# Performance work log

Hardware: AMD Instinct MI355X
Metric: run time of the kernel (lower is better)

Reference implementation:

```python
import jax, jax.numpy as jnp
import numpy as np

EPS = 1e-5
SCALE_MIN, SCALE_MAX = 0.6, 1.0


def _layer_norm(x):
    m = jnp.mean(x, axis=-1, keepdims=True)
    v = jnp.mean((x - m) ** 2, axis=-1, keepdims=True)
    return (x - m) / jnp.sqrt(v + EPS)


def _scan_dir(seq, A, Bp, Cp, D, W_in, W_out, snr_scale):
    """seq: [B, L, C] -> [B, L, C]. Diagonal SSM recurrence h = A*h + B*u."""
    Bsz, L, C = seq.shape
    N = A.shape[0]
    seq = _layer_norm(seq)
    u = jnp.einsum('blc,nc->bln', seq, W_in)                 # input_proj, [B,L,N]
    A_base = jnp.tanh(A)[None, :]                            # [1,N]
    s = jnp.clip(snr_scale, 0.0, 1.0)[:, None]               # [B,1]
    scale = SCALE_MIN + (SCALE_MAX - SCALE_MIN) * s
    Ad = jnp.clip(A_base * scale, -0.99, 0.99)               # [B,N]
    Bu = Bp[None, None, :] * u                               # [B,L,N]

    def step(h, bu_t):
        h = Ad * h + bu_t
        return h, h

    h0 = jnp.zeros((Bsz, N), dtype=seq.dtype)
    _, hs = jax.lax.scan(step, h0, jnp.swapaxes(Bu, 0, 1))   # hs: [L,B,N]
    hs = jnp.swapaxes(hs, 0, 1)                              # [B,L,N]
    y_state = Cp[None, None, :] * hs
    y = jnp.einsum('bln,cn->blc', y_state, W_out)            # output_proj
    return y + D[None, None, :] * seq


def _forward(x, snr_scale, A, Bparam, Cparam, D, W_in, W_out):
    Bsz, H, W, C = x.shape
    L = H * W
    if L > 4000:
        x = _layer_norm(x)
    # row scans
    seq_row = x.reshape(Bsz, L, C)
    y_row_f = _scan_dir(seq_row, A, Bparam, Cparam, D, W_in, W_out, snr_scale)
    y_row_b = _scan_dir(seq_row[:, ::-1, :], A, Bparam, Cparam, D, W_in, W_out, snr_scale)
    y_row = 0.5 * (y_row_f + y_row_b[:, ::-1, :])
    y_row = y_row.reshape(Bsz, H, W, C)
    # column scans
    x_col = jnp.transpose(x, (0, 2, 1, 3))                   # [B,W,H,C]
    seq_col = x_col.reshape(Bsz, L, C)
    y_col_f = _scan_dir(seq_col, A, Bparam, Cparam, D, W_in, W_out, snr_scale)
    y_col_b = _scan_dir(seq_col[:, ::-1, :], A, Bparam, Cparam, D, W_in, W_out, snr_scale)
    y_col = 0.5 * (y_col_f + y_col_b[:, ::-1, :])
    y_col = jnp.transpose(y_col.reshape(Bsz, W, H, C), (0, 2, 1, 3))
    return 0.5 * (y_row + y_col)


def setup_inputs() -> dict:
    key = jax.random.key(0)
    k = jax.random.split(key, 4)
    Bsz, H, W, C, N = 8, 64, 64, 256, 64
    x = jax.random.normal(k[0], (Bsz, H, W, C), dtype=jnp.float32)
    snr_scale = jax.random.uniform(k[1], (Bsz,), dtype=jnp.float32)
    A = -0.5 * jnp.ones((N,), dtype=jnp.float32)
    Bparam = 0.5 * jnp.ones((N,), dtype=jnp.float32)
    Cparam = 0.5 * jnp.ones((N,), dtype=jnp.float32)
    D = jnp.zeros((C,), dtype=jnp.float32)
    # nn.Linear default init: U(-1/sqrt(fan_in), 1/sqrt(fan_in))
    W_in = jax.random.uniform(k[2], (N, C), dtype=jnp.float32,
                              minval=-1.0 / np.sqrt(C), maxval=1.0 / np.sqrt(C))
    W_out = jax.random.uniform(k[3], (C, N), dtype=jnp.float32,
                               minval=-1.0 / np.sqrt(N), maxval=1.0 / np.sqrt(N))
    return {"x": x, "snr_scale": snr_scale, "A": A, "Bparam": Bparam,
            "Cparam": Cparam, "D": D, "W_in": W_in, "W_out": W_out}


def reference(x, snr_scale, A, Bparam, Cparam, D, W_in, W_out):
    return _forward(x, snr_scale, A, Bparam, Cparam, D, W_in, W_out)
```

## Files before the change

kernel.cpp:

```cpp
#include <hip/hip_runtime.h>
#include <hip/hip_bf16.h>
#include <math.h>

#define Bsz 8
#define Hh 64
#define Ww 64
#define Cc 256
#define Nn 64
#define Ll 4096
#define EPSf 1e-5f

typedef __bf16 v8bf __attribute__((ext_vector_type(8)));
typedef float  f32x4 __attribute__((ext_vector_type(4)));

__device__ __forceinline__ float ad_val(float a, float snr) {
    float s = fminf(fmaxf(snr, 0.f), 1.f);
    float scale = 0.6f + 0.4f * s;
    float v = tanhf(a) * scale;
    return fminf(fmaxf(v, -0.99f), 0.99f);
}

__global__ __launch_bounds__(256) void k0_weights(
    const float* __restrict__ Win, const float* __restrict__ Wout,
    const float* __restrict__ Bp, const float* __restrict__ Cp,
    __bf16* __restrict__ Wh, __bf16* __restrict__ Wl,
    __bf16* __restrict__ Woh, __bf16* __restrict__ Wol,
    float* __restrict__ WB)
{
    const int t = threadIdx.x;
    const int blk = blockIdx.x;
    if (blk < 4) {
        for (int idx = blk * 512 + t; idx < blk * 512 + 512; idx += 256) {
            int tile = idx >> 6, lane = idx & 63;
            int kt = tile >> 2, nt = tile & 3;
            int q = lane >> 4, n = nt * 16 + (lane & 15);
            #pragma unroll
            for (int j = 0; j < 8; ++j) {
                int k = kt * 32 + q * 8 + j;
                float w = Win[n * Cc + k];
                __bf16 h = (__bf16)w;
                Wh[idx * 8 + j] = h;
                Wl[idx * 8 + j] = (__bf16)(w - (float)h);
            }
        }
    } else if (blk < 8) {
        for (int idx = (blk - 4) * 512 + t; idx < (blk - 4) * 512 + 512; idx += 256) {
            int tile = idx >> 6, lane = idx & 63;
            int kt = tile >> 4, ntg = tile & 15;
            int q = lane >> 4, c = ntg * 16 + (lane & 15);
            #pragma unroll
            for (int j = 0; j < 8; ++j) {
                int k = kt * 32 + q * 8 + j;
                float w = Wout[c * Nn + k] * 0.25f * Cp[k];
                __bf16 h = (__bf16)w;
                Woh[idx * 8 + j] = h;
                Wol[idx * 8 + j] = (__bf16)(w - (float)h);
            }
        }
    } else {
        __shared__ float wtmp[256];
        int n = t >> 2, qd = t & 3;
        float s = 0.f;
        const float* wr = Win + (long)n * Cc + qd * 64;
        for (int i = 0; i < 64; ++i) s += wr[i];
        wtmp[t] = s;
        __syncthreads();
        if (t < 64)
            WB[t] = (wtmp[t*4] + wtmp[t*4+1] + wtmp[t*4+2] + wtmp[t*4+3]) * Bp[t];
    }
}

__global__ __launch_bounds__(256) void k1_ln_gemm(
    const float* __restrict__ x, const __bf16* __restrict__ Wh,
    const __bf16* __restrict__ Wl, const float* __restrict__ Bp,
    const float* __restrict__ WB, const float* __restrict__ A,
    const float* __restrict__ snr,
    float* __restrict__ Bu, float* __restrict__ E,
    float* __restrict__ Mst, float* __restrict__ Sst)
{
    __shared__ float tile[64 * 68];
    __shared__ float pfs[4][64], pbs[4][64];
    const int t = threadIdx.x;
    const int lane = t & 63;
    const int wv = __builtin_amdgcn_readfirstlane(t >> 6);
    const long pbase = (long)blockIdx.x * 64;
    const float* xt = x + pbase * Cc;

    const int q = lane >> 4;
    const int mi = lane & 15;
    const float* xa = xt + (long)(wv * 16 + mi) * Cc + q * 8;

    float4 axv[16];
    #pragma unroll
    for (int kt = 0; kt < 8; ++kt) {
        axv[kt * 2]     = *(const float4*)(xa + kt * 32);
        axv[kt * 2 + 1] = *(const float4*)(xa + kt * 32 + 4);
    }

    f32x4 acc[4];
    #pragma unroll
    for (int nt = 0; nt < 4; ++nt) acc[nt] = (f32x4){0.f, 0.f, 0.f, 0.f};
    float sacc = 0.f, qacc = 0.f;

    #pragma unroll
    for (int kt = 0; kt < 8; ++kt) {
        float4 a0 = axv[kt * 2];
        float4 a1 = axv[kt * 2 + 1];
        float av[8] = {a0.x, a0.y, a0.z, a0.w, a1.x, a1.y, a1.z, a1.w};
        v8bf ah, al;
        #pragma unroll
        for (int j = 0; j < 8; ++j) {
            sacc += av[j];
            qacc = fmaf(av[j], av[j], qacc);
            __bf16 h = (__bf16)av[j];
            ah[j] = h;
            al[j] = (__bf16)(av[j] - (float)h);
        }
        #pragma unroll
        for (int nt = 0; nt < 4; ++nt) {
            v8bf bh = *(const v8bf*)(Wh + ((long)(kt * 4 + nt) * 64 + lane) * 8);
            v8bf bl = *(const v8bf*)(Wl + ((long)(kt * 4 + nt) * 64 + lane) * 8);
            acc[nt] = __builtin_amdgcn_mfma_f32_16x16x32_bf16(ah, bh, acc[nt], 0, 0, 0);
            acc[nt] = __builtin_amdgcn_mfma_f32_16x16x32_bf16(al, bh, acc[nt], 0, 0, 0);
            acc[nt] = __builtin_amdgcn_mfma_f32_16x16x32_bf16(ah, bl, acc[nt], 0, 0, 0);
        }
    }

    sacc += __shfl_xor(sacc, 16);
    qacc += __shfl_xor(qacc, 16);
    sacc += __shfl_xor(sacc, 32);
    qacc += __shfl_xor(qacc, 32);
    float m_row = sacc * (1.f/256.f);
    float var = fmaxf(qacc * (1.f/256.f) - m_row * m_row, 0.f);
    float r1 = rsqrtf(var + EPSf);
    float v2 = var / (var + EPSf);
    float sc_row = r1 * rsqrtf(v2 + EPSf);
    if (lane < 16) {
        Mst[pbase + wv * 16 + mi] = m_row;
        Sst[pbase + wv * 16 + mi] = sc_row;
    }

    #pragma unroll
    for (int nt = 0; nt < 4; ++nt) {
        int n = nt * 16 + mi;
        float bpn = Bp[n];
        float wbn = WB[n];
        #pragma unroll
        for (int reg = 0; reg < 4; ++reg) {
            int p = wv * 16 + q * 4 + reg;
            float m = __shfl(m_row, q * 4 + reg);
            float s = __shfl(sc_row, q * 4 + reg);
            float val = s * (acc[nt][reg] * bpn - m * wbn);
            Bu[(pbase + p) * Nn + n] = val;
            tile[p * 68 + n] = val;
        }
    }
    __syncthreads();

    const int nn = t & 63;
    const int seg = t >> 6;
    const int bb = blockIdx.x >> 6;
    const int jj = blockIdx.x & 63;
    const float Adv = ad_val(A[nn], snr[bb]);

    float vv[16];
    #pragma unroll
    for (int k = 0; k < 16; ++k) vv[k] = tile[(seg * 16 + k) * 68 + nn];
    float f = 0.f, bw = 0.f;
    #pragma unroll
    for (int k = 0; k < 16; ++k) f = fmaf(Adv, f, vv[k]);
    #pragma unroll
    for (int k = 15; k >= 0; --k) bw = fmaf(Adv, bw, vv[k]);
    pfs[seg][nn] = f;
    pbs[seg][nn] = bw;
    __syncthreads();

    if (t < 64) {
        float Ad16 = Adv * Adv;
        Ad16 *= Ad16; Ad16 *= Ad16; Ad16 *= Ad16;
        float cf = pfs[0][t];
        #pragma unroll
        for (int i = 1; i < 4; ++i) cf = fmaf(Ad16, cf, pfs[i][t]);
        E[((0 * 8 + bb) * 64 + jj) * 64 + t] = cf;
        float cb = pbs[3][t];
        #pragma unroll
        for (int i = 2; i >= 0; --i) cb = fmaf(Ad16, cb, pbs[i][t]);
        E[((1 * 8 + bb) * 64 + (63 - jj)) * 64 + t] = cb;
    }
}

__global__ __launch_bounds__(64) void k2_carry(
    const float* __restrict__ Bu, const float* __restrict__ A,
    const float* __restrict__ snr, float* __restrict__ E)
{
    const int lane = threadIdx.x;
    const int task = blockIdx.x;
    const int b = (task >> 6) & 7;
    const int j = task & 63;
    const float Ad = ad_val(A[lane], snr[b]);
    const float* src = Bu + ((long)b * Ll + j) * Nn + lane;
    const long stride = (long)Ww * Nn;

    float v[64];
    #pragma unroll
    for (int k = 0; k < 64; ++k) v[k] = src[k * stride];

    float s = 0.f;
    #pragma unroll
    for (int k = 0; k < 64; ++k) s = fmaf(Ad, s, v[k]);
    E[((2 * 8 + b) * 64 + j) * 64 + lane] = s;

    float sb = 0.f;
    #pragma unroll
    for (int k = 63; k >= 0; --k) sb = fmaf(Ad, sb, v[k]);
    E[((3 * 8 + b) * 64 + (63 - j)) * 64 + lane] = sb;
}

__global__ __launch_bounds__(64) void k3_prefix(
    const float* __restrict__ E, float* __restrict__ CT,
    const float* __restrict__ A, const float* __restrict__ snr)
{
    const int lane = threadIdx.x;
    const int db = blockIdx.x;
    const int b = db & 7;
    float Ad = ad_val(A[lane], snr[b]);
    float p64 = Ad;
    #pragma unroll
    for (int i = 0; i < 6; ++i) p64 *= p64;
    const float* e = E + (long)db * 4096 + lane;
    float* ct = CT + (long)db * 4096 + lane;
    float v[64];
    #pragma unroll
    for (int k = 0; k < 64; ++k) v[k] = e[k * 64];
    float c = 0.f;
    #pragma unroll
    for (int k = 0; k < 64; ++k) {
        ct[k * 64] = c;
        c = fmaf(p64, c, v[k]);
    }
}

__global__ __launch_bounds__(64) void k4_apply(
    const float* __restrict__ Bu, const float* __restrict__ CT,
    const float* __restrict__ A, const float* __restrict__ snr,
    float* __restrict__ Scol)
{
    const int lane = threadIdx.x;
    const int task = blockIdx.x;
    const int b = (task >> 6) & 7;
    const int j = task & 63;
    const float Ad = ad_val(A[lane], snr[b]);
    const float* src = Bu + ((long)b * Ll + j) * Nn + lane;
    const long stride = (long)Ww * Nn;
    const float cf = CT[((2 * 8 + b) * 64 + j) * 64 + lane];
    const float cb = CT[((3 * 8 + b) * 64 + (63 - j)) * 64 + lane];

    float v[64];
    #pragma unroll
    for (int k = 0; k < 64; ++k) v[k] = src[k * stride];

    float hf[64];
    float h = cf;
    #pragma unroll
    for (int k = 0; k < 64; ++k) { h = fmaf(Ad, h, v[k]); hf[k] = h; }

    float* out0 = Scol + ((long)b * Ll + j) * Nn + lane;
    float sb = cb;
    #pragma unroll
    for (int k = 63; k >= 0; --k) {
        sb = fmaf(Ad, sb, v[k]);
        out0[k * stride] = hf[k] + sb;
    }
}

__global__ __launch_bounds__(256) void k5_gemm_out(
    const float* __restrict__ Bu, const float* __restrict__ Scol,
    const float* __restrict__ CT, const float* __restrict__ A,
    const float* __restrict__ snr,
    const float* __restrict__ x, const __bf16* __restrict__ Woh,
    const __bf16* __restrict__ Wol, const float* __restrict__ Dp,
    const float* __restrict__ Mst, const float* __restrict__ Sst,
    float* __restrict__ out)
{
    __shared__ float smem[64 * 260];
    __shared__ float pfs[4][64], pbs[4][64];
    const int t = threadIdx.x;
    const int lane = t & 63;
    const int wv = __builtin_amdgcn_readfirstlane(t >> 6);
    const long pbase = (long)blockIdx.x * 64;
    const int q = lane >> 4;
    const int mi = lane & 15;

    v8bf bh[2][4], bl[2][4];
    #pragma unroll
    for (int kt = 0; kt < 2; ++kt)
        #pragma unroll
        for (int nt = 0; nt < 4; ++nt) {
            long wo = ((long)(kt * 16 + wv * 4 + nt) * 64 + lane) * 8;
            bh[kt][nt] = *(const v8bf*)(Woh + wo);
            bl[kt][nt] = *(const v8bf*)(Wol + wo);
        }

    const int nn = t & 63;
    const int seg = wv;
    const int bb = blockIdx.x >> 6;
    const int jj = blockIdx.x & 63;
    const float Adv = ad_val(A[nn], snr[bb]);
    float Ad16 = Adv * Adv; Ad16 *= Ad16; Ad16 *= Ad16; Ad16 *= Ad16;
    const float cf  = CT[((0 * 8 + bb) * 64 + jj) * 64 + nn];
    const float cbg = CT[((1 * 8 + bb) * 64 + (63 - jj)) * 64 + nn];

    float vv[16], sc[16];
    const float* bup = Bu + (pbase + seg * 16) * Nn + nn;
    #pragma unroll
    for (int k = 0; k < 16; ++k) vv[k] = bup[k * 64];
    const float* scp = Scol + (pbase + seg * 16) * Nn + nn;
    #pragma unroll
    for (int k = 0; k < 16; ++k) sc[k] = scp[k * 64];

    float f = 0.f, bw = 0.f;
    #pragma unroll
    for (int k = 0; k < 16; ++k) f = fmaf(Adv, f, vv[k]);
    #pragma unroll
    for (int k = 15; k >= 0; --k) bw = fmaf(Adv, bw, vv[k]);
    pfs[seg][nn] = f;
    pbs[seg][nn] = bw;
    __syncthreads();

    float hseed = cf;
    for (int i = 0; i < seg; ++i) hseed = fmaf(Ad16, hseed, pfs[i][nn]);
    float bseed = cbg;
    for (int i = 3; i > seg; --i) bseed = fmaf(Ad16, bseed, pbs[i][nn]);

    float hf[16];
    float h = hseed;
    #pragma unroll
    for (int k = 0; k < 16; ++k) { h = fmaf(Adv, h, vv[k]); hf[k] = h; }
    float sb = bseed;
    #pragma unroll
    for (int k = 15; k >= 0; --k) {
        sb = fmaf(Adv, sb, vv[k]);
        smem[(seg * 16 + k) * 68 + nn] = hf[k] + sb + sc[k];
    }
    __syncthreads();

    f32x4 acc[4][4];
    #pragma unroll
    for (int mt = 0; mt < 4; ++mt)
        #pragma unroll
        for (int nt = 0; nt < 4; ++nt) acc[mt][nt] = (f32x4){0.f, 0.f, 0.f, 0.f};

    #pragma unroll
    for (int kt = 0; kt < 2; ++kt) {
        #pragma unroll
        for (int mt = 0; mt < 4; ++mt) {
            const float* ar = &smem[(mt * 16 + mi) * 68 + q * 8 + kt * 32];
            v8bf sh, sl;
            #pragma unroll
            for (int j = 0; j < 8; ++j) {
                float sv = ar[j];
                __bf16 hh = (__bf16)sv;
                sh[j] = hh;
                sl[j] = (__bf16)(sv - (float)hh);
            }
            #pragma unroll
            for (int nt = 0; nt < 4; ++nt) {
                acc[mt][nt] = __builtin_amdgcn_mfma_f32_16x16x32_bf16(sh, bh[kt][nt], acc[mt][nt], 0, 0, 0);
                acc[mt][nt] = __builtin_amdgcn_mfma_f32_16x16x32_bf16(sl, bh[kt][nt], acc[mt][nt], 0, 0, 0);
                acc[mt][nt] = __builtin_amdgcn_mfma_f32_16x16x32_bf16(sh, bl[kt][nt], acc[mt][nt], 0, 0, 0);
            }
        }
    }
    __syncthreads();
    #pragma unroll
    for (int mt = 0; mt < 4; ++mt)
        #pragma unroll
        for (int nt = 0; nt < 4; ++nt) {
            int c = wv * 64 + nt * 16 + mi;
            #pragma unroll
            for (int reg = 0; reg < 4; ++reg)
                smem[(mt * 16 + q * 4 + reg) * 260 + c] = acc[mt][nt][reg];
        }
    __syncthreads();

    const float4* xg = (const float4*)(x + pbase * Cc);
    float4* og = (float4*)(out + pbase * Cc);
    const float4 dv = ((const float4*)Dp)[lane];
    #pragma unroll 4
    for (int i = 0; i < 16; ++i) {
        int fi = i * 256 + t;
        int p = i * 4 + wv;
        float4 v = *(const float4*)&smem[p * 260 + lane * 4];
        float m = Mst[pbase + p], s = Sst[pbase + p];
        float4 xv = xg[fi];
        og[fi] = make_float4(v.x + dv.x * ((xv.x - m) * s),
                             v.y + dv.y * ((xv.y - m) * s),
                             v.z + dv.z * ((xv.z - m) * s),
                             v.w + dv.w * ((xv.w - m) * s));
    }
}

extern "C" void kernel_launch(void* const* d_in, const int* in_sizes, int n_in,
                              void* d_out, int out_size, void* d_ws, size_t ws_size,
                              hipStream_t stream)
{
    const float* x    = (const float*)d_in[0];
    const float* snr  = (const float*)d_in[1];
    const float* A    = (const float*)d_in[2];
    const float* Bp   = (const float*)d_in[3];
    const float* Cp   = (const float*)d_in[4];
    const float* Dp   = (const float*)d_in[5];
    const float* Win  = (const float*)d_in[6];
    const float* Wout = (const float*)d_in[7];
    float* out = (float*)d_out;

    char* ws = (char*)d_ws;
    float*  Bu   = (float*)(ws);
    float*  Scol = (float*)(ws + (size_t)8  * 1024 * 1024);
    float*  E    = (float*)(ws + (size_t)16 * 1024 * 1024);
    float*  CT   = (float*)(ws + (size_t)16 * 1024 * 1024 + 512*1024);
    float*  Mst  = (float*)(ws + (size_t)17 * 1024 * 1024);
    float*  Sst  = (float*)(ws + (size_t)17 * 1024 * 1024 + 128*1024);
    char*   wbase = ws + (size_t)17 * 1024 * 1024 + 512 * 1024;
    __bf16* Wh   = (__bf16*)(wbase);
    __bf16* Wl   = (__bf16*)(wbase + 32 * 1024);
    __bf16* Woh  = (__bf16*)(wbase + 64 * 1024);
    __bf16* Wol  = (__bf16*)(wbase + 96 * 1024);
    float*  WB   = (float*)(wbase + 128 * 1024);

    hipLaunchKernelGGL(k0_weights,  dim3(9),   dim3(256), 0, stream, Win, Wout, Bp, Cp, Wh, Wl, Woh, Wol, WB);
    hipLaunchKernelGGL(k1_ln_gemm,  dim3(512), dim3(256), 0, stream, x, Wh, Wl, Bp, WB, A, snr, Bu, E, Mst, Sst);
    hipLaunchKernelGGL(k2_carry,    dim3(512), dim3(64),  0, stream, Bu, A, snr, E);
    hipLaunchKernelGGL(k3_prefix,   dim3(32),  dim3(64),  0, stream, E, CT, A, snr);
    hipLaunchKernelGGL(k4_apply,    dim3(512), dim3(64),  0, stream, Bu, CT, A, snr, Scol);
    hipLaunchKernelGGL(k5_gemm_out, dim3(512), dim3(256), 0, stream, Bu, Scol, CT, A, snr, x, Woh, Wol, Dp, Mst, Sst, out);
}
```

Baseline: 128.9 us.

## Fuse six kernels into one cooperative kernel with grid-wide syncs

Merges the weight-prep, LN+GEMM, carry, prefix, apply and output GEMM stages into a single cooperative launch of 512 blocks, separated by grid.sync barriers. It removes per-kernel launch gaps and tail idle time between the six dependent stages. In exchange every stage now runs at 256 threads even where only 64 are used (carry, apply), grid syncs add barrier cost, and occupancy is capped by launch_bounds(256,2) plus the large shared array. The old multi-kernel path is kept as a fallback if the cooperative launch is unavailable.

```diff
diff --git a/kernel.cpp b/kernel.cpp
--- a/kernel.cpp
+++ b/kernel.cpp
@@ -1,6 +1,9 @@
 #include <hip/hip_runtime.h>
+#include <hip/hip_cooperative_groups.h>
 #include <hip/hip_bf16.h>
 #include <math.h>
+
+namespace cg = cooperative_groups;
 
 #define Bsz 8
 #define Hh 64
@@ -19,6 +22,7 @@
     float v = tanhf(a) * scale;
     return fminf(fmaxf(v, -0.99f), 0.99f);
 }
+
 
 __global__ __launch_bounds__(256) void k0_weights(
     const float* __restrict__ Win, const float* __restrict__ Wout,
@@ -400,6 +404,361 @@
     }
 }
 
+__global__ __launch_bounds__(256, 2) void mega(
+    const float* __restrict__ x, const float* __restrict__ snr,
+    const float* __restrict__ A, const float* __restrict__ Bp,
+    const float* __restrict__ Cp, const float* __restrict__ Dp,
+    const float* __restrict__ Win, const float* __restrict__ Wout,
+    __bf16* __restrict__ Wh, __bf16* __restrict__ Wl,
+    __bf16* __restrict__ Woh, __bf16* __restrict__ Wol,
+    float* __restrict__ WB,
+    float* __restrict__ Bu, float* __restrict__ Scol,
+    float* __restrict__ E, float* __restrict__ CT,
+    float* __restrict__ Mst, float* __restrict__ Sst,
+    float* __restrict__ out)
+{
+    cg::grid_group grid = cg::this_grid();
+    __shared__ float smem[64 * 260];
+    __shared__ float pfs[4][64], pbs[4][64];
+    const int t = threadIdx.x;
+    const int lane = t & 63;
+    const int wv = __builtin_amdgcn_readfirstlane(t >> 6);
+    const int blk = blockIdx.x;
+    const long pbase = (long)blk * 64;
+    const int q = lane >> 4;
+    const int mi = lane & 15;
+    const int nn = t & 63;
+    const int bb = blk >> 6;
+    const int jj = blk & 63;
+
+    if (blk < 4) {
+        for (int idx = blk * 512 + t; idx < blk * 512 + 512; idx += 256) {
+            int tile = idx >> 6, ln = idx & 63;
+            int kt = tile >> 2, nt = tile & 3;
+            int qq = ln >> 4, n = nt * 16 + (ln & 15);
+            #pragma unroll
+            for (int j = 0; j < 8; ++j) {
+                int k = kt * 32 + qq * 8 + j;
+                float w = Win[n * Cc + k];
+                __bf16 h = (__bf16)w;
+                Wh[idx * 8 + j] = h;
+                Wl[idx * 8 + j] = (__bf16)(w - (float)h);
+            }
+        }
+    } else if (blk < 8) {
+        for (int idx = (blk - 4) * 512 + t; idx < (blk - 4) * 512 + 512; idx += 256) {
+            int tile = idx >> 6, ln = idx & 63;
+            int kt = tile >> 4, ntg = tile & 15;
+            int qq = ln >> 4, c = ntg * 16 + (ln & 15);
+            #pragma unroll
+            for (int j = 0; j < 8; ++j) {
+                int k = kt * 32 + qq * 8 + j;
+                float w = Wout[c * Nn + k] * 0.25f * Cp[k];
+                __bf16 h = (__bf16)w;
+                Woh[idx * 8 + j] = h;
+                Wol[idx * 8 + j] = (__bf16)(w - (float)h);
+            }
+        }
+    } else if (blk == 8) {
+        float* wtmp = smem;
+        int n = t >> 2, qd = t & 3;
+        float s = 0.f;
+        const float* wr = Win + (long)n * Cc + qd * 64;
+        for (int i = 0; i < 64; ++i) s += wr[i];
+        wtmp[t] = s;
+        __syncthreads();
+        if (t < 64)
+            WB[t] = (wtmp[t*4] + wtmp[t*4+1] + wtmp[t*4+2] + wtmp[t*4+3]) * Bp[t];
+        __syncthreads();
+    }
+    __threadfence();
+    grid.sync();
+
+    {
+        float* tile = smem;
+        const float* xt = x + pbase * Cc;
+        const float* xa = xt + (long)(wv * 16 + mi) * Cc + q * 8;
+
+        float4 axv[16];
+        #pragma unroll
+        for (int kt = 0; kt < 8; ++kt) {
+            axv[kt * 2]     = *(const float4*)(xa + kt * 32);
+            axv[kt * 2 + 1] = *(const float4*)(xa + kt * 32 + 4);
+        }
+
+        f32x4 acc[4];
+        #pragma unroll
+        for (int nt = 0; nt < 4; ++nt) acc[nt] = (f32x4){0.f, 0.f, 0.f, 0.f};
+        float sacc = 0.f, qacc = 0.f;
+
+        #pragma unroll
+        for (int kt = 0; kt < 8; ++kt) {
+            float4 a0 = axv[kt * 2];
+            float4 a1 = axv[kt * 2 + 1];
+            float av[8] = {a0.x, a0.y, a0.z, a0.w, a1.x, a1.y, a1.z, a1.w};
+            v8bf ah, al;
+            #pragma unroll
+            for (int j = 0; j < 8; ++j) {
+                sacc += av[j];
+                qacc = fmaf(av[j], av[j], qacc);
+                __bf16 h = (__bf16)av[j];
+                ah[j] = h;
+                al[j] = (__bf16)(av[j] - (float)h);
+            }
+            #pragma unroll
+            for (int nt = 0; nt < 4; ++nt) {
+                v8bf bh = *(const v8bf*)(Wh + ((long)(kt * 4 + nt) * 64 + lane) * 8);
+                v8bf bl = *(const v8bf*)(Wl + ((long)(kt * 4 + nt) * 64 + lane) * 8);
+                acc[nt] = __builtin_amdgcn_mfma_f32_16x16x32_bf16(ah, bh, acc[nt], 0, 0, 0);
+                acc[nt] = __builtin_amdgcn_mfma_f32_16x16x32_bf16(al, bh, acc[nt], 0, 0, 0);
+                acc[nt] = __builtin_amdgcn_mfma_f32_16x16x32_bf16(ah, bl, acc[nt], 0, 0, 0);
+            }
+        }
+
+        sacc += __shfl_xor(sacc, 16);
+        qacc += __shfl_xor(qacc, 16);
+        sacc += __shfl_xor(sacc, 32);
+        qacc += __shfl_xor(qacc, 32);
+        float m_row = sacc * (1.f/256.f);
+        float var = fmaxf(qacc * (1.f/256.f) - m_row * m_row, 0.f);
+        float r1 = rsqrtf(var + EPSf);
+        float v2 = var / (var + EPSf);
+        float sc_row = r1 * rsqrtf(v2 + EPSf);
+        if (lane < 16) {
+            Mst[pbase + wv * 16 + mi] = m_row;
+            Sst[pbase + wv * 16 + mi] = sc_row;
+        }
+
+        #pragma unroll
+        for (int nt = 0; nt < 4; ++nt) {
+            int n = nt * 16 + mi;
+            float bpn = Bp[n];
+            float wbn = WB[n];
+            #pragma unroll
+            for (int reg = 0; reg < 4; ++reg) {
+                int p = wv * 16 + q * 4 + reg;
+                float m = __shfl(m_row, q * 4 + reg);
+                float s = __shfl(sc_row, q * 4 + reg);
+                float val = s * (acc[nt][reg] * bpn - m * wbn);
+                Bu[(pbase + p) * Nn + n] = val;
+                tile[p * 68 + n] = val;
+            }
+        }
+        __syncthreads();
+
+        const int seg = t >> 6;
+        const float Adv = ad_val(A[nn], snr[bb]);
+        float vv[16];
+        #pragma unroll
+        for (int k = 0; k < 16; ++k) vv[k] = tile[(seg * 16 + k) * 68 + nn];
+        float f = 0.f, bw = 0.f;
+        #pragma unroll
+        for (int k = 0; k < 16; ++k) f = fmaf(Adv, f, vv[k]);
+        #pragma unroll
+        for (int k = 15; k >= 0; --k) bw = fmaf(Adv, bw, vv[k]);
+        pfs[seg][nn] = f;
+        pbs[seg][nn] = bw;
+        __syncthreads();
+
+        if (t < 64) {
+            float Ad16 = Adv * Adv;
+            Ad16 *= Ad16; Ad16 *= Ad16; Ad16 *= Ad16;
+            float cf = pfs[0][t];
+            #pragma unroll
+            for (int i = 1; i < 4; ++i) cf = fmaf(Ad16, cf, pfs[i][t]);
+            E[((0 * 8 + bb) * 64 + jj) * 64 + t] = cf;
+            float cb = pbs[3][t];
+            #pragma unroll
+            for (int i = 2; i >= 0; --i) cb = fmaf(Ad16, cb, pbs[i][t]);
+            E[((1 * 8 + bb) * 64 + (63 - jj)) * 64 + t] = cb;
+        }
+    }
+    __threadfence();
+    grid.sync();
+
+    if (t < 64) {
+        const int b = (blk >> 6) & 7;
+        const int j = blk & 63;
+        const float Ad = ad_val(A[t], snr[b]);
+        const float* src = Bu + ((long)b * Ll + j) * Nn + t;
+        const long stride = (long)Ww * Nn;
+
+        float v[64];
+        #pragma unroll
+        for (int k = 0; k < 64; ++k) v[k] = src[k * stride];
+
+        float s = 0.f;
+        #pragma unroll
+        for (int k = 0; k < 64; ++k) s = fmaf(Ad, s, v[k]);
+        E[((2 * 8 + b) * 64 + j) * 64 + t] = s;
+
+        float sb = 0.f;
+        #pragma unroll
+        for (int k = 63; k >= 0; --k) sb = fmaf(Ad, sb, v[k]);
+        E[((3 * 8 + b) * 64 + (63 - j)) * 64 + t] = sb;
+    }
+    __threadfence();
+    grid.sync();
+
+    if (blk < 32 && t < 64) {
+        const int db = blk;
+        const int b = db & 7;
+        float Ad = ad_val(A[t], snr[b]);
+        float p64 = Ad;
+        #pragma unroll
+        for (int i = 0; i < 6; ++i) p64 *= p64;
+        const float* e = E + (long)db * 4096 + t;
+        float* ct = CT + (long)db * 4096 + t;
+        float v[64];
+        #pragma unroll
+        for (int k = 0; k < 64; ++k) v[k] = e[k * 64];
+        float c = 0.f;
+        #pragma unroll
+        for (int k = 0; k < 64; ++k) {
+            ct[k * 64] = c;
+            c = fmaf(p64, c, v[k]);
+        }
+    }
+    __threadfence();
+    grid.sync();
+
+    if (t < 64) {
+        const int b = (blk >> 6) & 7;
+        const int j = blk & 63;
+        const float Ad = ad_val(A[t], snr[b]);
+        const float* src = Bu + ((long)b * Ll + j) * Nn + t;
+        const long stride = (long)Ww * Nn;
+        const float cf = CT[((2 * 8 + b) * 64 + j) * 64 + t];
+        const float cb = CT[((3 * 8 + b) * 64 + (63 - j)) * 64 + t];
+
+        float v[64];
+        #pragma unroll
+        for (int k = 0; k < 64; ++k) v[k] = src[k * stride];
+
+        float hf[64];
+        float h = cf;
+        #pragma unroll
+        for (int k = 0; k < 64; ++k) { h = fmaf(Ad, h, v[k]); hf[k] = h; }
+
+        float* out0 = Scol + ((long)b * Ll + j) * Nn + t;
+        float sb = cb;
+        #pragma unroll
+        for (int k = 63; k >= 0; --k) {
+            sb = fmaf(Ad, sb, v[k]);
+            out0[k * stride] = hf[k] + sb;
+        }
+    }
+    __threadfence();
+    grid.sync();
+
+    {
+        v8bf bh[2][4], bl[2][4];
+        #pragma unroll
+        for (int kt = 0; kt < 2; ++kt)
+            #pragma unroll
+            for (int nt = 0; nt < 4; ++nt) {
+                long wo = ((long)(kt * 16 + wv * 4 + nt) * 64 + lane) * 8;
+                bh[kt][nt] = *(const v8bf*)(Woh + wo);
+                bl[kt][nt] = *(const v8bf*)(Wol + wo);
+            }
+
+        const int seg = wv;
+        const float Adv = ad_val(A[nn], snr[bb]);
+        float Ad16 = Adv * Adv; Ad16 *= Ad16; Ad16 *= Ad16; Ad16 *= Ad16;
+        const float cf  = CT[((0 * 8 + bb) * 64 + jj) * 64 + nn];
+        const float cbg = CT[((1 * 8 + bb) * 64 + (63 - jj)) * 64 + nn];
+
+        float vv[16], sc[16];
+        const float* bup = Bu + (pbase + seg * 16) * Nn + nn;
+        #pragma unroll
+        for (int k = 0; k < 16; ++k) vv[k] = bup[k * 64];
+        const float* scp = Scol + (pbase + seg * 16) * Nn + nn;
+        #pragma unroll
+        for (int k = 0; k < 16; ++k) sc[k] = scp[k * 64];
+
+        float f = 0.f, bw = 0.f;
+        #pragma unroll
+        for (int k = 0; k < 16; ++k) f = fmaf(Adv, f, vv[k]);
+        #pragma unroll
+        for (int k = 15; k >= 0; --k) bw = fmaf(Adv, bw, vv[k]);
+        pfs[seg][nn] = f;
+        pbs[seg][nn] = bw;
+        __syncthreads();
+
+        float hseed = cf;
+        for (int i = 0; i < seg; ++i) hseed = fmaf(Ad16, hseed, pfs[i][nn]);
+        float bseed = cbg;
+        for (int i = 3; i > seg; --i) bseed = fmaf(Ad16, bseed, pbs[i][nn]);
+
+        float hf[16];
+        float h = hseed;
+        #pragma unroll
+        for (int k = 0; k < 16; ++k) { h = fmaf(Adv, h, vv[k]); hf[k] = h; }
+        float sb = bseed;
+        #pragma unroll
+        for (int k = 15; k >= 0; --k) {
+            sb = fmaf(Adv, sb, vv[k]);
+            smem[(seg * 16 + k) * 68 + nn] = hf[k] + sb + sc[k];
+        }
+        __syncthreads();
+
+        f32x4 acc[4][4];
+        #pragma unroll
+        for (int mt = 0; mt < 4; ++mt)
+            #pragma unroll
+            for (int nt = 0; nt < 4; ++nt) acc[mt][nt] = (f32x4){0.f, 0.f, 0.f, 0.f};
+
+        #pragma unroll
+        for (int kt = 0; kt < 2; ++kt) {
+            #pragma unroll
+            for (int mt = 0; mt < 4; ++mt) {
+                const float* ar = &smem[(mt * 16 + mi) * 68 + q * 8 + kt * 32];
+                v8bf sh, sl;
+                #pragma unroll
+                for (int j = 0; j < 8; ++j) {
+                    float sv = ar[j];
+                    __bf16 hh = (__bf16)sv;
+                    sh[j] = hh;
+                    sl[j] = (__bf16)(sv - (float)hh);
+                }
+                #pragma unroll
+                for (int nt = 0; nt < 4; ++nt) {
+                    acc[mt][nt] = __builtin_amdgcn_mfma_f32_16x16x32_bf16(sh, bh[kt][nt], acc[mt][nt], 0, 0, 0);
+                    acc[mt][nt] = __builtin_amdgcn_mfma_f32_16x16x32_bf16(sl, bh[kt][nt], acc[mt][nt], 0, 0, 0);
+                    acc[mt][nt] = __builtin_amdgcn_mfma_f32_16x16x32_bf16(sh, bl[kt][nt], acc[mt][nt], 0, 0, 0);
+                }
+            }
+        }
+        __syncthreads();
+        #pragma unroll
+        for (int mt = 0; mt < 4; ++mt)
+            #pragma unroll
+            for (int nt = 0; nt < 4; ++nt) {
+                int c = wv * 64 + nt * 16 + mi;
+                #pragma unroll
+                for (int reg = 0; reg < 4; ++reg)
+                    smem[(mt * 16 + q * 4 + reg) * 260 + c] = acc[mt][nt][reg];
+            }
+        __syncthreads();
+
+        const float4* xg = (const float4*)(x + pbase * Cc);
+        float4* og = (float4*)(out + pbase * Cc);
+        const float4 dv = ((const float4*)Dp)[lane];
+        #pragma unroll 4
+        for (int i = 0; i < 16; ++i) {
+            int fi = i * 256 + t;
+            int p = i * 4 + wv;
+            float4 v = *(const float4*)&smem[p * 260 + lane * 4];
+            float m = Mst[pbase + p], s = Sst[pbase + p];
+            float4 xv = xg[fi];
+            og[fi] = make_float4(v.x + dv.x * ((xv.x - m) * s),
+                                 v.y + dv.y * ((xv.y - m) * s),
+                                 v.z + dv.z * ((xv.z - m) * s),
+                                 v.w + dv.w * ((xv.w - m) * s));
+        }
+    }
+}
+
 extern "C" void kernel_launch(void* const* d_in, const int* in_sizes, int n_in,
                               void* d_out, int out_size, void* d_ws, size_t ws_size,
                               hipStream_t stream)
@@ -428,10 +787,28 @@
     __bf16* Wol  = (__bf16*)(wbase + 96 * 1024);
     float*  WB   = (float*)(wbase + 128 * 1024);
 
-    hipLaunchKernelGGL(k0_weights,  dim3(9),   dim3(256), 0, stream, Win, Wout, Bp, Cp, Wh, Wl, Woh, Wol, WB);
-    hipLaunchKernelGGL(k1_ln_gemm,  dim3(512), dim3(256), 0, stream, x, Wh, Wl, Bp, WB, A, snr, Bu, E, Mst, Sst);
-    hipLaunchKernelGGL(k2_carry,    dim3(512), dim3(64),  0, stream, Bu, A, snr, E);
-    hipLaunchKernelGGL(k3_prefix,   dim3(32),  dim3(64),  0, stream, E, CT, A, snr);
-    hipLaunchKernelGGL(k4_apply,    dim3(512), dim3(64),  0, stream, Bu, CT, A, snr, Scol);
-    hipLaunchKernelGGL(k5_gemm_out, dim3(512), dim3(256), 0, stream, Bu, Scol, CT, A, snr, x, Woh, Wol, Dp, Mst, Sst, out);
+    int maxActive = 0;
+    hipError_t occErr = hipOccupancyMaxActiveBlocksPerMultiprocessor(
+        &maxActive, reinterpret_cast<const void*>(mega), 256, 0);
+    hipError_t lerr = hipErrorUnknown;
+    if (occErr == hipSuccess && maxActive >= 2) {
+        void* args[] = {
+            (void*)&x, (void*)&snr, (void*)&A, (void*)&Bp, (void*)&Cp,
+            (void*)&Dp, (void*)&Win, (void*)&Wout,
+            (void*)&Wh, (void*)&Wl, (void*)&Woh, (void*)&Wol, (void*)&WB,
+            (void*)&Bu, (void*)&Scol, (void*)&E, (void*)&CT,
+            (void*)&Mst, (void*)&Sst, (void*)&out
+        };
+        lerr = hipLaunchCooperativeKernel(reinterpret_cast<void*>(mega),
+                                          dim3(512), dim3(256), args, 0, stream);
+    }
+    if (lerr != hipSuccess) {
+        (void)hipGetLastError();
+        hipLaunchKernelGGL(k0_weights,  dim3(9),   dim3(256), 0, stream, Win, Wout, Bp, Cp, Wh, Wl, Woh, Wol, WB);
+        hipLaunchKernelGGL(k1_ln_gemm,  dim3(512), dim3(256), 0, stream, x, Wh, Wl, Bp, WB, A, snr, Bu, E, Mst, Sst);
+        hipLaunchKernelGGL(k2_carry,    dim3(512), dim3(64),  0, stream, Bu, A, snr, E);
+        hipLaunchKernelGGL(k3_prefix,   dim3(32),  dim3(64),  0, stream, E, CT, A, snr);
+        hipLaunchKernelGGL(k4_apply,    dim3(512), dim3(64),  0, stream, Bu, CT, A, snr, Scol);
+        hipLaunchKernelGGL(k5_gemm_out, dim3(512), dim3(256), 0, stream, Bu, Scol, CT, A, snr, x, Woh, Wol, Dp, Mst, Sst, out);
+    }
 }
```

Measured after the change: 127.5 us. About the same (-1.1%).
